# Performance work log

Hardware: AMD Instinct MI355X
Metric: run time of the kernel (lower is better)

The kernel has to match this reference:

```python
import jax, jax.numpy as jnp
import numpy as np

N_BINS = 10  # init default of ECELoss


def setup_inputs() -> dict:
    key = jax.random.key(0)
    k1, k2 = jax.random.split(key)
    N, C = 2_000_000, 100
    raw = jax.random.normal(k1, (N, C), dtype=jnp.float32)
    # module computes exp(logits) and expects confidences in (0, 1],
    # so the logits it receives are log-probabilities
    logits = jax.nn.log_softmax(raw, axis=1)
    labels = jax.random.randint(k2, (N,), 0, C, dtype=jnp.int64)
    return {"logits": logits, "labels": labels}


def reference(logits, labels):
    softmaxes = jnp.exp(logits)                       # [N, C]
    confidences = jnp.max(softmaxes, axis=1)          # [N]
    predictions = jnp.argmax(softmaxes, axis=1)       # [N]
    accuracies = (predictions == labels).astype(jnp.float32)

    n = confidences.shape[0]
    # bin i holds conf in (i/n_bins, (i+1)/n_bins]  ->  ceil(conf*n_bins)-1
    bin_idx = jnp.ceil(confidences * N_BINS).astype(jnp.int32) - 1
    # conf <= 0 belongs to no bin (strict lower bound on bin 0); conf > 1
    # already maps to an out-of-range index. Out-of-range ids are dropped
    # by segment_sum.
    bin_idx = jnp.where(confidences <= 0.0, N_BINS, bin_idx)

    ones = jnp.ones_like(confidences)
    counts = jax.ops.segment_sum(ones, bin_idx, num_segments=N_BINS)
    sum_conf = jax.ops.segment_sum(confidences, bin_idx, num_segments=N_BINS)
    sum_acc = jax.ops.segment_sum(accuracies, bin_idx, num_segments=N_BINS)

    prop_in_bin = counts / n
    safe = jnp.maximum(counts, 1.0)
    gap = jnp.abs(sum_conf / safe - sum_acc / safe)
    ece = jnp.sum(jnp.where(counts > 0, gap * prop_in_bin, 0.0))
    return ece.reshape(1)
```

## Files before the change

kernel.cpp:

```cpp
#include <hip/hip_runtime.h>
#include <math.h>

#define NBINS 10
#define MAIN_BLOCKS 2048
#define MAIN_THREADS 256
#define NV4 25


__global__ void ece_zero_ws(float* ws) {
    int i = threadIdx.x;
    if (i < 3 * NBINS) ws[i] = 0.0f;
}

__global__ __launch_bounds__(MAIN_THREADS) void ece_main(
        const float* __restrict__ logits,
        const int* __restrict__ labels,
        float* __restrict__ ws,
        int N) {
    __shared__ float sbin[3 * NBINS];
    const int tid = threadIdx.x;
    if (tid < 3 * NBINS) sbin[tid] = 0.0f;
    __syncthreads();

    const float4* __restrict__ lg4 = (const float4*)logits;
    const long long stride = (long long)gridDim.x * MAIN_THREADS;
    long long row = (long long)blockIdx.x * MAIN_THREADS + tid;

    for (; row < (long long)N; row += stride) {
        const float4* __restrict__ rp = lg4 + row * NV4;

        float4 v[NV4];
        #pragma unroll
        for (int j = 0; j < NV4; ++j) v[j] = rp[j];

        float m = -INFINITY;
        int midx = 0;
        #pragma unroll
        for (int j = 0; j < NV4; ++j) {
            const int e = 4 * j;
            if (v[j].x > m) { m = v[j].x; midx = e; }
            if (v[j].y > m) { m = v[j].y; midx = e + 1; }
            if (v[j].z > m) { m = v[j].z; midx = e + 2; }
            if (v[j].w > m) { m = v[j].w; midx = e + 3; }
        }

        const float conf = expf(m);
        const int b = (int)ceilf(conf * 10.0f) - 1;
        const float acc = (midx == labels[row]) ? 1.0f : 0.0f;
        if (b >= 0 && b < NBINS) {
            atomicAdd(&sbin[b], 1.0f);
            atomicAdd(&sbin[NBINS + b], conf);
            atomicAdd(&sbin[2 * NBINS + b], acc);
        }
    }

    __syncthreads();
    if (tid < 3 * NBINS) {
        const float s = sbin[tid];
        if (s != 0.0f) atomicAdd(&ws[tid], s);
    }
}

__global__ void ece_final(const float* __restrict__ ws, float* __restrict__ out, int N) {
    if (threadIdx.x == 0 && blockIdx.x == 0) {
        float ece = 0.0f;
        for (int b = 0; b < NBINS; ++b) {
            const float cnt = ws[b];
            if (cnt > 0.0f) {
                const float avg_conf = ws[NBINS + b] / cnt;
                const float avg_acc  = ws[2 * NBINS + b] / cnt;
                ece += fabsf(avg_conf - avg_acc) * (cnt / (float)N);
            }
        }
        out[0] = ece;
    }
}

extern "C" void kernel_launch(void* const* d_in, const int* in_sizes, int n_in,
                              void* d_out, int out_size, void* d_ws, size_t ws_size,
                              hipStream_t stream) {
    const float* logits = (const float*)d_in[0];
    const int*   labels = (const int*)d_in[1];
    float* out = (float*)d_out;
    float* ws  = (float*)d_ws;

    const int N = in_sizes[1];

    ece_zero_ws<<<1, 64, 0, stream>>>(ws);
    ece_main<<<MAIN_BLOCKS, MAIN_THREADS, 0, stream>>>(logits, labels, ws, N);
    ece_final<<<1, 64, 0, stream>>>(ws, out, N);
}
```

Baseline: 1.019 ms.

## Stage row tiles into LDS with direct global-to-LDS coalesced loads

```diff
diff --git a/kernel.cpp b/kernel.cpp
--- a/kernel.cpp
+++ b/kernel.cpp
@@ -2,9 +2,12 @@
 #include <math.h>
 
 #define NBINS 10
-#define MAIN_BLOCKS 2048
-#define MAIN_THREADS 256
-#define NV4 25
+#define BLOCKS 768
+#define THREADS 128
+#define TILE_ROWS 64
+#define ROW_F4 25
+#define TILE_F4 (TILE_ROWS * ROW_F4)
+#define LOADS_PER_LANE 25
 
 
 __global__ void ece_zero_ws(float* ws) {
@@ -12,45 +15,69 @@
     if (i < 3 * NBINS) ws[i] = 0.0f;
 }
 
-__global__ __launch_bounds__(MAIN_THREADS) void ece_main(
+__global__ __launch_bounds__(THREADS) void ece_main(
         const float* __restrict__ logits,
         const int* __restrict__ labels,
         float* __restrict__ ws,
         int N) {
+    __shared__ __align__(16) float tile[2][TILE_ROWS * 100];
     __shared__ float sbin[3 * NBINS];
     const int tid = threadIdx.x;
     if (tid < 3 * NBINS) sbin[tid] = 0.0f;
     __syncthreads();
 
-    const float4* __restrict__ lg4 = (const float4*)logits;
-    const long long stride = (long long)gridDim.x * MAIN_THREADS;
-    long long row = (long long)blockIdx.x * MAIN_THREADS + tid;
+    const int lane = tid & 63;
+    const int w = tid >> 6;
+    float* const mybuf = &tile[w][0];
 
-    for (; row < (long long)N; row += stride) {
-        const float4* __restrict__ rp = lg4 + row * NV4;
+    const long long nTiles = ((long long)N + TILE_ROWS - 1) / TILE_ROWS;
+    const long long waveId = (long long)blockIdx.x * 2 + w;
+    const long long nWaves = (long long)gridDim.x * 2;
 
-        float4 v[NV4];
+    const float4* const lg4 = (const float4*)logits;
+    const long long lastF4 = (long long)N * ROW_F4 - 1;
+
+    typedef const __attribute__((address_space(1))) void* gptr_t;
+    typedef __attribute__((address_space(3))) void* lptr_t;
+
+    for (long long t = waveId; t < nTiles; t += nWaves) {
+        const long long base_f4 = t * (long long)TILE_F4;
+
+        asm volatile("s_waitcnt lgkmcnt(0)" ::: "memory");
+
         #pragma unroll
-        for (int j = 0; j < NV4; ++j) v[j] = rp[j];
+        for (int j = 0; j < LOADS_PER_LANE; ++j) {
+            long long g = base_f4 + j * 64 + lane;
+            if (g > lastF4) g = lastF4;
+            __builtin_amdgcn_global_load_lds(
+                (gptr_t)(lg4 + g),
+                (lptr_t)(mybuf + j * 256),
+                16, 0, 0);
+        }
+        asm volatile("s_waitcnt vmcnt(0)" ::: "memory");
 
-        float m = -INFINITY;
-        int midx = 0;
-        #pragma unroll
-        for (int j = 0; j < NV4; ++j) {
-            const int e = 4 * j;
-            if (v[j].x > m) { m = v[j].x; midx = e; }
-            if (v[j].y > m) { m = v[j].y; midx = e + 1; }
-            if (v[j].z > m) { m = v[j].z; midx = e + 2; }
-            if (v[j].w > m) { m = v[j].w; midx = e + 3; }
-        }
-
-        const float conf = expf(m);
-        const int b = (int)ceilf(conf * 10.0f) - 1;
-        const float acc = (midx == labels[row]) ? 1.0f : 0.0f;
-        if (b >= 0 && b < NBINS) {
-            atomicAdd(&sbin[b], 1.0f);
-            atomicAdd(&sbin[NBINS + b], conf);
-            atomicAdd(&sbin[2 * NBINS + b], acc);
+        const long long row = t * TILE_ROWS + lane;
+        if (row < (long long)N) {
+            const float4* const rp = (const float4*)(mybuf + lane * 100);
+            float m = -INFINITY;
+            int midx = 0;
+            #pragma unroll
+            for (int j = 0; j < ROW_F4; ++j) {
+                const float4 v = rp[j];
+                const int e = 4 * j;
+                if (v.x > m) { m = v.x; midx = e; }
+                if (v.y > m) { m = v.y; midx = e + 1; }
+                if (v.z > m) { m = v.z; midx = e + 2; }
+                if (v.w > m) { m = v.w; midx = e + 3; }
+            }
+            const float conf = expf(m);
+            const int b = (int)ceilf(conf * 10.0f) - 1;
+            const float acc = (midx == labels[row]) ? 1.0f : 0.0f;
+            if (b >= 0 && b < NBINS) {
+                atomicAdd(&sbin[b], 1.0f);
+                atomicAdd(&sbin[NBINS + b], conf);
+                atomicAdd(&sbin[2 * NBINS + b], acc);
+            }
         }
     }
 
@@ -87,6 +114,6 @@
     const int N = in_sizes[1];
 
     ece_zero_ws<<<1, 64, 0, stream>>>(ws);
-    ece_main<<<MAIN_BLOCKS, MAIN_THREADS, 0, stream>>>(logits, labels, ws, N);
+    ece_main<<<BLOCKS, THREADS, 0, stream>>>(logits, labels, ws, N);
     ece_final<<<1, 64, 0, stream>>>(ws, out, N);
 }
```

Measured after the change: 993.9 us. -2.4%, faster.
